# Kernel tuning notes

Measured on AMD Instinct MI355X. Metric: run time of the kernel, lower is better.

## Reference

```python
import math
import jax, jax.numpy as jnp
import numpy as np

B, S, D, L = 8, 4096, 1024, 16

def setup_inputs() -> dict:
    key = jax.random.key(0)
    k1, k2, k3 = jax.random.split(key, 3)
    memory = jax.random.normal(k1, (B, S, D), dtype=jnp.float32)
    summarizer = jax.random.normal(k2, (L, D), dtype=jnp.float32) * 0.02
    w_proj = jax.random.normal(k3, (1, L), dtype=jnp.float32) * (1.0 / math.sqrt(L))
    return {"memory": memory, "summarizer": summarizer, "w_proj": w_proj}

def reference(memory, summarizer, w_proj):
    # scores: [B, L, S] = summarizer @ memory^T / sqrt(D)
    d = summarizer.shape[-1]
    scores = jnp.einsum('ld,bsd->bls', summarizer, memory) / jnp.sqrt(jnp.asarray(d, memory.dtype))
    p_attn = jax.nn.softmax(scores, axis=-1)            # softmax over sequence S
    ctx = jnp.einsum('bls,bsd->bld', p_attn, memory)    # [B, L, D]
    # nn.Linear(L, 1, bias=False) applied to ctx.transpose(-1,-2): [B, D, L] @ W^T -> [B, D, 1]
    out = jnp.einsum('bld,l->bd', ctx, w_proj[0])       # [B, D]
    return out[:, None, :]                              # [B, 1, D] after final transpose
```

## Files before the change

### kernel.cpp

```cpp
#include <hip/hip_runtime.h>
#include <hip/hip_bf16.h>

#define BB 8
#define SS 4096
#define DD 1024
#define LL 16
#define SPAD 1032

typedef __attribute__((ext_vector_type(8))) short short8;
typedef __attribute__((ext_vector_type(4))) float fl4;

static __device__ __forceinline__ short f2bf(float f) {
    unsigned u = __float_as_uint(f);
    u += 0x7FFFu + ((u >> 16) & 1u);
    return (short)(u >> 16);
}

__global__ __launch_bounds__(256) void k_fused(const float* __restrict__ mem,
                                               const float* __restrict__ summ,
                                               float* __restrict__ part,
                                               float* __restrict__ Zpart) {
    __shared__ short summ_l[LL * SPAD];
    __shared__ float e_lds[64 * LL];
    __shared__ float zp[4][LL];

    int blk = blockIdx.x;
    int b   = blk >> 6;
    int s0  = (blk & 63) << 6;
    int t    = threadIdx.x;
    int w    = t >> 6;
    int lane = t & 63;
    int o  = lane & 15;
    int qd = lane >> 4;

    for (int i = t; i < LL * DD / 4; i += 256) {
        int l = i >> 8, d = (i & 255) * 4;
        fl4 v = *(const fl4*)(summ + l * DD + d);
        short tmp[4];
        tmp[0] = f2bf(v[0]); tmp[1] = f2bf(v[1]);
        tmp[2] = f2bf(v[2]); tmp[3] = f2bf(v[3]);
        *(unsigned long long*)&summ_l[l * SPAD + d] = *(unsigned long long*)tmp;
    }
    __syncthreads();

    const short* arow = summ_l + o * SPAD + qd * 8;
    const float* mrow = mem + ((size_t)b * SS + s0 + w * 16 + o) * DD + qd * 8;

    fl4 acc = {0.f, 0.f, 0.f, 0.f};
    #pragma unroll 8
    for (int k = 0; k < DD; k += 32) {
        short8 a = *(const short8*)(arow + k);
        fl4 f0 = *(const fl4*)(mrow + k);
        fl4 f1 = *(const fl4*)(mrow + k + 4);
        short8 bb;
        bb[0] = f2bf(f0[0]); bb[1] = f2bf(f0[1]);
        bb[2] = f2bf(f0[2]); bb[3] = f2bf(f0[3]);
        bb[4] = f2bf(f1[0]); bb[5] = f2bf(f1[1]);
        bb[6] = f2bf(f1[2]); bb[7] = f2bf(f1[3]);
        acc = __builtin_amdgcn_mfma_f32_16x16x32_bf16(a, bb, acc, 0, 0, 0);
    }

    const float scale = 0.03125f;
    fl4 ev;
    #pragma unroll
    for (int r = 0; r < 4; ++r) ev[r] = __expf(acc[r] * scale);
    *(fl4*)&e_lds[(w * 16 + o) * LL + qd * 4] = ev;

    fl4 zs = ev;
    #pragma unroll
    for (int r = 0; r < 4; ++r) {
        float v = zs[r];
        v += __shfl_xor(v, 1, 64);
        v += __shfl_xor(v, 2, 64);
        v += __shfl_xor(v, 4, 64);
        v += __shfl_xor(v, 8, 64);
        zs[r] = v;
    }
    if (o == 0) *(fl4*)&zp[w][qd * 4] = zs;
    __syncthreads();

    fl4 ctx[LL];
    #pragma unroll
    for (int l = 0; l < LL; ++l) ctx[l] = (fl4){0.f, 0.f, 0.f, 0.f};
    const float* mb = mem + ((size_t)b * SS + s0) * DD + t * 4;
    #pragma unroll 4
    for (int s = 0; s < 64; ++s) {
        fl4 m4 = *(const fl4*)(mb + (size_t)s * DD);
        const fl4* ee = (const fl4*)&e_lds[s * LL];
        #pragma unroll
        for (int g = 0; g < 4; ++g) {
            fl4 e4 = ee[g];
            ctx[g * 4 + 0] += e4[0] * m4;
            ctx[g * 4 + 1] += e4[1] * m4;
            ctx[g * 4 + 2] += e4[2] * m4;
            ctx[g * 4 + 3] += e4[3] * m4;
        }
    }
    float* pp = part + (size_t)blk * LL * DD + t * 4;
    #pragma unroll
    for (int l = 0; l < LL; ++l) *(fl4*)(pp + l * DD) = ctx[l];
    if (t < LL) Zpart[blk * LL + t] = zp[0][t] + zp[1][t] + zp[2][t] + zp[3][t];
}

__global__ __launch_bounds__(256) void k_out(const float* __restrict__ part,
                                             const float* __restrict__ Zpart,
                                             const float* __restrict__ w,
                                             float* __restrict__ out) {
    int blkid = blockIdx.x;
    int b  = blkid >> 4;
    int d0 = (blkid & 15) << 6;
    int t = threadIdx.x;
    __shared__ float zz[16][LL];
    __shared__ float coef[LL];
    __shared__ float red[4][64];

    int l = t & 15, cq = t >> 4;
    float zsum = 0.f;
    #pragma unroll
    for (int j = 0; j < 4; ++j) zsum += Zpart[(b * 64 + cq * 4 + j) * LL + l];
    zz[cq][l] = zsum;
    __syncthreads();
    if (t < LL) {
        float Z = 0.f;
        #pragma unroll
        for (int g = 0; g < 16; ++g) Z += zz[g][t];
        coef[t] = w[t] / Z;
    }
    __syncthreads();

    float c[LL];
    #pragma unroll
    for (int i = 0; i < LL; ++i) c[i] = coef[i];
    int doff = t & 63, cg = t >> 6;
    float accv = 0.f;
    for (int ch = cg * 16; ch < cg * 16 + 16; ++ch) {
        const float* pb = part + (size_t)(b * 64 + ch) * LL * DD + d0 + doff;
        #pragma unroll
        for (int l2 = 0; l2 < LL; ++l2) accv += c[l2] * pb[(size_t)l2 * DD];
    }
    red[cg][doff] = accv;
    __syncthreads();
    if (t < 64) out[b * DD + d0 + t] = red[0][t] + red[1][t] + red[2][t] + red[3][t];
}

extern "C" void kernel_launch(void* const* d_in, const int* in_sizes, int n_in,
                              void* d_out, int out_size, void* d_ws, size_t ws_size,
                              hipStream_t stream) {
    const float* mem  = (const float*)d_in[0];
    const float* summ = (const float*)d_in[1];
    const float* w    = (const float*)d_in[2];
    float* out = (float*)d_out;

    char* ws = (char*)d_ws;
    float* Zpart = (float*)ws;
    float* part  = (float*)(ws + 64 * 1024);

    k_fused<<<BB * 64, 256, 0, stream>>>(mem, summ, part, Zpart);
    k_out<<<BB * 16, 256, 0, stream>>>(part, Zpart, w, out);
}
```

Measured before the change: 237.3 us.

## Fold output projection into softmax weights and fuse into one cooperative kernel

Instead of building a per-block partial context tensor [L,D] and reducing it in a second kernel, the softmax denominators are gathered with a grid-wide sync. Each block then collapses its 16 attention rows into one weight per position using w/Z and does a single weighted sum over memory, accumulated into the output with atomics. This removes the 16x context FMA work and the large partial-buffer write and read, at the cost of a cooperative launch, a grid barrier, and float atomics with nondeterministic summation order.

```diff
diff --git a/kernel.cpp b/kernel.cpp
--- a/kernel.cpp
+++ b/kernel.cpp
@@ -1,5 +1,8 @@
 #include <hip/hip_runtime.h>
 #include <hip/hip_bf16.h>
+#include <hip/hip_cooperative_groups.h>
+
+namespace cg = cooperative_groups;
 
 #define BB 8
 #define SS 4096
@@ -16,19 +19,23 @@
     return (short)(u >> 16);
 }
 
-__global__ __launch_bounds__(256) void k_fused(const float* __restrict__ mem,
-                                               const float* __restrict__ summ,
-                                               float* __restrict__ part,
-                                               float* __restrict__ Zpart) {
+__global__ __launch_bounds__(256) void k_all(const float* __restrict__ mem,
+                                             const float* __restrict__ summ,
+                                             const float* __restrict__ w,
+                                             float* __restrict__ out,
+                                             float* __restrict__ Zpart) {
     __shared__ short summ_l[LL * SPAD];
     __shared__ float e_lds[64 * LL];
     __shared__ float zp[4][LL];
+    __shared__ float zz[16][LL];
+    __shared__ float coef[LL];
+    __shared__ float qs[64];
 
     int blk = blockIdx.x;
     int b   = blk >> 6;
     int s0  = (blk & 63) << 6;
     int t    = threadIdx.x;
-    int w    = t >> 6;
+    int wv   = t >> 6;
     int lane = t & 63;
     int o  = lane & 15;
     int qd = lane >> 4;
@@ -41,10 +48,13 @@
         tmp[2] = f2bf(v[2]); tmp[3] = f2bf(v[3]);
         *(unsigned long long*)&summ_l[l * SPAD + d] = *(unsigned long long*)tmp;
     }
+    if (blk == 0) {
+        for (int i = t; i < BB * DD; i += 256) out[i] = 0.f;
+    }
     __syncthreads();
 
     const short* arow = summ_l + o * SPAD + qd * 8;
-    const float* mrow = mem + ((size_t)b * SS + s0 + w * 16 + o) * DD + qd * 8;
+    const float* mrow = mem + ((size_t)b * SS + s0 + wv * 16 + o) * DD + qd * 8;
 
     fl4 acc = {0.f, 0.f, 0.f, 0.f};
     #pragma unroll 8
@@ -64,7 +74,7 @@
     fl4 ev;
     #pragma unroll
     for (int r = 0; r < 4; ++r) ev[r] = __expf(acc[r] * scale);
-    *(fl4*)&e_lds[(w * 16 + o) * LL + qd * 4] = ev;
+    *(fl4*)&e_lds[(wv * 16 + o) * LL + qd * 4] = ev;
 
     fl4 zs = ev;
     #pragma unroll
@@ -76,71 +86,49 @@
         v += __shfl_xor(v, 8, 64);
         zs[r] = v;
     }
-    if (o == 0) *(fl4*)&zp[w][qd * 4] = zs;
+    if (o == 0) *(fl4*)&zp[wv][qd * 4] = zs;
     __syncthreads();
+    if (t < LL) Zpart[blk * LL + t] = zp[0][t] + zp[1][t] + zp[2][t] + zp[3][t];
 
-    fl4 ctx[LL];
-    #pragma unroll
-    for (int l = 0; l < LL; ++l) ctx[l] = (fl4){0.f, 0.f, 0.f, 0.f};
-    const float* mb = mem + ((size_t)b * SS + s0) * DD + t * 4;
-    #pragma unroll 4
-    for (int s = 0; s < 64; ++s) {
-        fl4 m4 = *(const fl4*)(mb + (size_t)s * DD);
-        const fl4* ee = (const fl4*)&e_lds[s * LL];
+    __threadfence();
+    cg::this_grid().sync();
+
+    {
+        int l = t & 15, g = t >> 4;
+        float zsum = 0.f;
         #pragma unroll
-        for (int g = 0; g < 4; ++g) {
-            fl4 e4 = ee[g];
-            ctx[g * 4 + 0] += e4[0] * m4;
-            ctx[g * 4 + 1] += e4[1] * m4;
-            ctx[g * 4 + 2] += e4[2] * m4;
-            ctx[g * 4 + 3] += e4[3] * m4;
-        }
+        for (int j = 0; j < 4; ++j) zsum += Zpart[(b * 64 + g * 4 + j) * LL + l];
+        zz[g][l] = zsum;
     }
-    float* pp = part + (size_t)blk * LL * DD + t * 4;
-    #pragma unroll
-    for (int l = 0; l < LL; ++l) *(fl4*)(pp + l * DD) = ctx[l];
-    if (t < LL) Zpart[blk * LL + t] = zp[0][t] + zp[1][t] + zp[2][t] + zp[3][t];
-}
-
-__global__ __launch_bounds__(256) void k_out(const float* __restrict__ part,
-                                             const float* __restrict__ Zpart,
-                                             const float* __restrict__ w,
-                                             float* __restrict__ out) {
-    int blkid = blockIdx.x;
-    int b  = blkid >> 4;
-    int d0 = (blkid & 15) << 6;
-    int t = threadIdx.x;
-    __shared__ float zz[16][LL];
-    __shared__ float coef[LL];
-    __shared__ float red[4][64];
-
-    int l = t & 15, cq = t >> 4;
-    float zsum = 0.f;
-    #pragma unroll
-    for (int j = 0; j < 4; ++j) zsum += Zpart[(b * 64 + cq * 4 + j) * LL + l];
-    zz[cq][l] = zsum;
     __syncthreads();
     if (t < LL) {
-        float Z = 0.f;
+        float Zt = 0.f;
         #pragma unroll
-        for (int g = 0; g < 16; ++g) Z += zz[g][t];
-        coef[t] = w[t] / Z;
+        for (int g = 0; g < 16; ++g) Zt += zz[g][t];
+        coef[t] = w[t] / Zt;
+    }
+    __syncthreads();
+    if (t < 64) {
+        const float* ep = &e_lds[t * LL];
+        float qv = 0.f;
+        #pragma unroll
+        for (int l = 0; l < LL; ++l) qv += coef[l] * ep[l];
+        qs[t] = qv;
     }
     __syncthreads();
 
-    float c[LL];
-    #pragma unroll
-    for (int i = 0; i < LL; ++i) c[i] = coef[i];
-    int doff = t & 63, cg = t >> 6;
-    float accv = 0.f;
-    for (int ch = cg * 16; ch < cg * 16 + 16; ++ch) {
-        const float* pb = part + (size_t)(b * 64 + ch) * LL * DD + d0 + doff;
-        #pragma unroll
-        for (int l2 = 0; l2 < LL; ++l2) accv += c[l2] * pb[(size_t)l2 * DD];
+    const float* mb = mem + ((size_t)b * SS + s0) * DD + t * 4;
+    fl4 cacc = {0.f, 0.f, 0.f, 0.f};
+    #pragma unroll 8
+    for (int i = 0; i < 64; ++i) {
+        fl4 m4 = *(const fl4*)(mb + (size_t)i * DD);
+        cacc += qs[i] * m4;
     }
-    red[cg][doff] = accv;
-    __syncthreads();
-    if (t < 64) out[b * DD + d0 + t] = red[0][t] + red[1][t] + red[2][t] + red[3][t];
+    float* op = out + (size_t)b * DD + t * 4;
+    atomicAdd(op + 0, cacc[0]);
+    atomicAdd(op + 1, cacc[1]);
+    atomicAdd(op + 2, cacc[2]);
+    atomicAdd(op + 3, cacc[3]);
 }
 
 extern "C" void kernel_launch(void* const* d_in, const int* in_sizes, int n_in,
@@ -150,11 +138,9 @@
     const float* summ = (const float*)d_in[1];
     const float* w    = (const float*)d_in[2];
     float* out = (float*)d_out;
+    float* Zpart = (float*)d_ws;
 
-    char* ws = (char*)d_ws;
-    float* Zpart = (float*)ws;
-    float* part  = (float*)(ws + 64 * 1024);
-
-    k_fused<<<BB * 64, 256, 0, stream>>>(mem, summ, part, Zpart);
-    k_out<<<BB * 16, 256, 0, stream>>>(part, Zpart, w, out);
+    void* args[] = {(void*)&mem, (void*)&summ, (void*)&w, (void*)&out, (void*)&Zpart};
+    hipLaunchCooperativeKernel((const void*)k_all, dim3(BB * 64), dim3(256),
+                               args, 0, stream);
 }
```

After: 320.1 us. +34.9%, slower.

## Stage memory rows into LDS with double-buffered async DMA and single global read

Applied to the files above, without the earlier changes.

Rewrites the main kernel so each block processes 128 sequence rows in 16-row steps, loading them into double-buffered LDS via global_load_lds so the score MFMA and context accumulation both read from LDS instead of reading memory twice from global. Summarizer fragments are kept in registers, split across waves by D quarter, and reduced through LDS. Grid halves to 256 blocks, and the reduction kernel is adjusted to the new partition count. The large LDS footprint limits occupancy to one block per CU, and more barriers are added per step.

```diff
diff --git a/kernel.cpp b/kernel.cpp
--- a/kernel.cpp
+++ b/kernel.cpp
@@ -5,7 +5,7 @@
 #define SS 4096
 #define DD 1024
 #define LL 16
-#define SPAD 1032
+#define ROWF 1028
 
 typedef __attribute__((ext_vector_type(8))) short short8;
 typedef __attribute__((ext_vector_type(4))) float fl4;
@@ -16,90 +16,141 @@
     return (short)(u >> 16);
 }
 
-__global__ __launch_bounds__(256) void k_fused(const float* __restrict__ mem,
-                                               const float* __restrict__ summ,
-                                               float* __restrict__ part,
-                                               float* __restrict__ Zpart) {
-    __shared__ short summ_l[LL * SPAD];
-    __shared__ float e_lds[64 * LL];
-    __shared__ float zp[4][LL];
+static __device__ __forceinline__ short8 pack8(fl4 a, fl4 b) {
+    short8 r;
+    r[0] = f2bf(a[0]); r[1] = f2bf(a[1]); r[2] = f2bf(a[2]); r[3] = f2bf(a[3]);
+    r[4] = f2bf(b[0]); r[5] = f2bf(b[1]); r[6] = f2bf(b[2]); r[7] = f2bf(b[3]);
+    return r;
+}
+
+static __device__ __forceinline__ void dma16(const float* g, float* l) {
+    __builtin_amdgcn_global_load_lds(
+        (const __attribute__((address_space(1))) void*)g,
+        (__attribute__((address_space(3))) void*)l, 16, 0, 0);
+}
+
+__global__ __launch_bounds__(256) void k_main(const float* __restrict__ mem,
+                                              const float* __restrict__ summ,
+                                              float* __restrict__ part,
+                                              float* __restrict__ Zpart) {
+    __shared__ float buf[2][16 * ROWF];
+    __shared__ float e_lds[16 * LL];
+    __shared__ float scr[4][256];
 
     int blk = blockIdx.x;
-    int b   = blk >> 6;
-    int s0  = (blk & 63) << 6;
+    int b   = blk >> 5;
+    int s_base = (blk & 31) << 7;
     int t    = threadIdx.x;
-    int w    = t >> 6;
+    int wv   = t >> 6;
     int lane = t & 63;
     int o  = lane & 15;
     int qd = lane >> 4;
 
-    for (int i = t; i < LL * DD / 4; i += 256) {
-        int l = i >> 8, d = (i & 255) * 4;
-        fl4 v = *(const fl4*)(summ + l * DD + d);
-        short tmp[4];
-        tmp[0] = f2bf(v[0]); tmp[1] = f2bf(v[1]);
-        tmp[2] = f2bf(v[2]); tmp[3] = f2bf(v[3]);
-        *(unsigned long long*)&summ_l[l * SPAD + d] = *(unsigned long long*)tmp;
-    }
-    __syncthreads();
-
-    const short* arow = summ_l + o * SPAD + qd * 8;
-    const float* mrow = mem + ((size_t)b * SS + s0 + w * 16 + o) * DD + qd * 8;
-
-    fl4 acc = {0.f, 0.f, 0.f, 0.f};
-    #pragma unroll 8
-    for (int k = 0; k < DD; k += 32) {
-        short8 a = *(const short8*)(arow + k);
-        fl4 f0 = *(const fl4*)(mrow + k);
-        fl4 f1 = *(const fl4*)(mrow + k + 4);
-        short8 bb;
-        bb[0] = f2bf(f0[0]); bb[1] = f2bf(f0[1]);
-        bb[2] = f2bf(f0[2]); bb[3] = f2bf(f0[3]);
-        bb[4] = f2bf(f1[0]); bb[5] = f2bf(f1[1]);
-        bb[6] = f2bf(f1[2]); bb[7] = f2bf(f1[3]);
-        acc = __builtin_amdgcn_mfma_f32_16x16x32_bf16(a, bb, acc, 0, 0, 0);
-    }
-
-    const float scale = 0.03125f;
-    fl4 ev;
-    #pragma unroll
-    for (int r = 0; r < 4; ++r) ev[r] = __expf(acc[r] * scale);
-    *(fl4*)&e_lds[(w * 16 + o) * LL + qd * 4] = ev;
-
-    fl4 zs = ev;
+    short8 afr[8];
+    {
+        const float* arow = summ + o * DD + wv * 256 + qd * 8;
+        #pragma unroll
+        for (int j = 0; j < 8; ++j) {
+            fl4 a0 = *(const fl4*)(arow + j * 32);
+            fl4 a1 = *(const fl4*)(arow + j * 32 + 4);
+            afr[j] = pack8(a0, a1);
+        }
+    }
+
+    const float* gseg = mem + ((size_t)b * SS + s_base) * DD;
+
     #pragma unroll
     for (int r = 0; r < 4; ++r) {
-        float v = zs[r];
-        v += __shfl_xor(v, 1, 64);
-        v += __shfl_xor(v, 2, 64);
-        v += __shfl_xor(v, 4, 64);
-        v += __shfl_xor(v, 8, 64);
-        zs[r] = v;
-    }
-    if (o == 0) *(fl4*)&zp[w][qd * 4] = zs;
-    __syncthreads();
+        int row = wv * 4 + r;
+        #pragma unroll
+        for (int c = 0; c < 4; ++c)
+            dma16(gseg + (size_t)row * DD + c * 256 + lane * 4,
+                  &buf[0][row * ROWF + c * 256]);
+    }
 
     fl4 ctx[LL];
     #pragma unroll
     for (int l = 0; l < LL; ++l) ctx[l] = (fl4){0.f, 0.f, 0.f, 0.f};
-    const float* mb = mem + ((size_t)b * SS + s0) * DD + t * 4;
-    #pragma unroll 4
-    for (int s = 0; s < 64; ++s) {
-        fl4 m4 = *(const fl4*)(mb + (size_t)s * DD);
-        const fl4* ee = (const fl4*)&e_lds[s * LL];
-        #pragma unroll
-        for (int g = 0; g < 4; ++g) {
-            fl4 e4 = ee[g];
-            ctx[g * 4 + 0] += e4[0] * m4;
-            ctx[g * 4 + 1] += e4[1] * m4;
-            ctx[g * 4 + 2] += e4[2] * m4;
-            ctx[g * 4 + 3] += e4[3] * m4;
-        }
-    }
+    fl4 zacc = {0.f, 0.f, 0.f, 0.f};
+    const float scale = 0.03125f;
+
+    for (int p = 0; p < 8; ++p) {
+        __syncthreads();
+        if (p < 7) {
+            float* nbuf = &buf[(p + 1) & 1][0];
+            const float* gp = gseg + (size_t)(p + 1) * 16 * DD;
+            #pragma unroll
+            for (int r = 0; r < 4; ++r) {
+                int row = wv * 4 + r;
+                #pragma unroll
+                for (int c = 0; c < 4; ++c)
+                    dma16(gp + (size_t)row * DD + c * 256 + lane * 4,
+                          &nbuf[row * ROWF + c * 256]);
+            }
+            asm volatile("s_waitcnt vmcnt(16)" ::: "memory");
+        } else {
+            asm volatile("s_waitcnt vmcnt(0)" ::: "memory");
+        }
+        __syncthreads();
+
+        const float* bbase = &buf[p & 1][0];
+        fl4 acc = {0.f, 0.f, 0.f, 0.f};
+        const float* brow = bbase + o * ROWF + wv * 256 + qd * 8;
+        #pragma unroll
+        for (int j = 0; j < 8; ++j) {
+            fl4 f0 = *(const fl4*)(brow + j * 32);
+            fl4 f1 = *(const fl4*)(brow + j * 32 + 4);
+            acc = __builtin_amdgcn_mfma_f32_16x16x32_bf16(afr[j], pack8(f0, f1),
+                                                          acc, 0, 0, 0);
+        }
+        *(fl4*)&scr[wv][lane * 4] = acc;
+        __syncthreads();
+        if (wv == 0) {
+            fl4 s0 = *(const fl4*)&scr[0][lane * 4];
+            fl4 s1 = *(const fl4*)&scr[1][lane * 4];
+            fl4 s2 = *(const fl4*)&scr[2][lane * 4];
+            fl4 s3 = *(const fl4*)&scr[3][lane * 4];
+            fl4 ev;
+            #pragma unroll
+            for (int r = 0; r < 4; ++r)
+                ev[r] = __expf((s0[r] + s1[r] + s2[r] + s3[r]) * scale);
+            *(fl4*)&e_lds[o * LL + qd * 4] = ev;
+            zacc += ev;
+        }
+        __syncthreads();
+
+        const float* mrow = bbase + t * 4;
+        #pragma unroll 4
+        for (int s = 0; s < 16; ++s) {
+            fl4 m4 = *(const fl4*)(mrow + s * ROWF);
+            const fl4* ee = (const fl4*)&e_lds[s * LL];
+            #pragma unroll
+            for (int g = 0; g < 4; ++g) {
+                fl4 e4 = ee[g];
+                ctx[g * 4 + 0] += e4[0] * m4;
+                ctx[g * 4 + 1] += e4[1] * m4;
+                ctx[g * 4 + 2] += e4[2] * m4;
+                ctx[g * 4 + 3] += e4[3] * m4;
+            }
+        }
+    }
+
     float* pp = part + (size_t)blk * LL * DD + t * 4;
     #pragma unroll
-    for (int l = 0; l < LL; ++l) *(fl4*)(pp + l * DD) = ctx[l];
-    if (t < LL) Zpart[blk * LL + t] = zp[0][t] + zp[1][t] + zp[2][t] + zp[3][t];
+    for (int l = 0; l < LL; ++l) *(fl4*)(pp + (size_t)l * DD) = ctx[l];
+
+    if (wv == 0) {
+        #pragma unroll
+        for (int r = 0; r < 4; ++r) {
+            float v = zacc[r];
+            v += __shfl_xor(v, 1, 64);
+            v += __shfl_xor(v, 2, 64);
+            v += __shfl_xor(v, 4, 64);
+            v += __shfl_xor(v, 8, 64);
+            zacc[r] = v;
+        }
+        if (o == 0) *(fl4*)&Zpart[blk * LL + qd * 4] = zacc;
+    }
 }
 
 __global__ __launch_bounds__(256) void k_out(const float* __restrict__ part,
@@ -110,35 +161,25 @@
     int b  = blkid >> 4;
     int d0 = (blkid & 15) << 6;
     int t = threadIdx.x;
-    __shared__ float zz[16][LL];
     __shared__ float coef[LL];
     __shared__ float red[4][64];
 
-    int l = t & 15, cq = t >> 4;
-    float zsum = 0.f;
-    #pragma unroll
-    for (int j = 0; j < 4; ++j) zsum += Zpart[(b * 64 + cq * 4 + j) * LL + l];
-    zz[cq][l] = zsum;
-    __syncthreads();
     if (t < LL) {
         float Z = 0.f;
         #pragma unroll
-        for (int g = 0; g < 16; ++g) Z += zz[g][t];
+        for (int s = 0; s < 32; ++s) Z += Zpart[(b * 32 + s) * LL + t];
         coef[t] = w[t] / Z;
     }
     __syncthreads();
 
-    float c[LL];
-    #pragma unroll
-    for (int i = 0; i < LL; ++i) c[i] = coef[i];
-    int doff = t & 63, cg = t >> 6;
-    float accv = 0.f;
-    for (int ch = cg * 16; ch < cg * 16 + 16; ++ch) {
-        const float* pb = part + (size_t)(b * 64 + ch) * LL * DD + d0 + doff;
-        #pragma unroll
-        for (int l2 = 0; l2 < LL; ++l2) accv += c[l2] * pb[(size_t)l2 * DD];
-    }
-    red[cg][doff] = accv;
+    int dd = t & 63, cg = t >> 6;
+    float acc = 0.f;
+    for (int seg = cg * 8; seg < cg * 8 + 8; ++seg) {
+        const float* pb = part + (size_t)(b * 32 + seg) * LL * DD + d0 + dd;
+        #pragma unroll
+        for (int l = 0; l < LL; ++l) acc += coef[l] * pb[(size_t)l * DD];
+    }
+    red[cg][dd] = acc;
     __syncthreads();
     if (t < 64) out[b * DD + d0 + t] = red[0][t] + red[1][t] + red[2][t] + red[3][t];
 }
@@ -155,6 +196,6 @@
     float* Zpart = (float*)ws;
     float* part  = (float*)(ws + 64 * 1024);
 
-    k_fused<<<BB * 64, 256, 0, stream>>>(mem, summ, part, Zpart);
-    k_out<<<BB * 16, 256, 0, stream>>>(part, Zpart, w, out);
-}
+    k_main<<<256, 256, 0, stream>>>(mem, summ, part, Zpart);
+    k_out<<<128, 256, 0, stream>>>(part, Zpart, w, out);
+}
```

After: 208.6 us. 12.1% less time.
